# Optimization experiments

Measured on AMD Instinct MI355X. Metric: run time of the kernel, lower is better.

The kernel has to match this reference:

```python
import jax, jax.numpy as jnp
import numpy as np

B, D, T, H, OUT = 256, 256, 256, 512, 256

def setup_inputs() -> dict:
    key = jax.random.key(0)
    ks = jax.random.split(key, 7)
    s = lambda fan: 1.0 / np.sqrt(fan)
    x = jax.random.normal(ks[0], (B, D, T), dtype=jnp.float32)
    Wx = jax.random.normal(ks[1], (D, H), dtype=jnp.float32) * s(D)
    Wh = jax.random.normal(ks[2], (H, H), dtype=jnp.float32) * s(H)
    b = jnp.zeros((H,), dtype=jnp.float32)
    Wout = jax.random.normal(ks[3], (H, OUT), dtype=jnp.float32) * s(H)
    bout = jnp.zeros((OUT,), dtype=jnp.float32)
    init_state = jnp.zeros((1, H), dtype=jnp.float32)  # non-trainable zeros in keras
    return {"x": x, "Wx": Wx, "Wh": Wh, "b": b, "Wout": Wout, "bout": bout, "init_state": init_state}

def reference(x, Wx, Wh, b, Wout, bout, init_state):
    # x: [B, D, T] (time on last axis, as unstacked in the keras layer)
    batch = x.shape[0]
    h0 = jnp.tile(init_state, (batch, 1))              # [B, H]
    xs = jnp.moveaxis(x, -1, 0)                        # [T, B, D]
    # precompute input projections for all steps (hoisted out of the recurrence)
    xproj = jnp.einsum('tbd,dh->tbh', xs, Wx) + b      # [T, B, H]

    def step(h_prev, xp):
        cur = jnp.tanh(xp + h_prev @ Wh)
        # residual: state_i = cell_out + state_{i-1}; at i=0 h_prev is zeros, so always adding is exact
        new = cur + h_prev
        return new, new

    _, states = jax.lax.scan(step, h0, xproj)          # states: [T, B, H]
    states = jnp.moveaxis(states, 0, 1)                # [B, T, H]
    out = states @ Wout + bout                         # [B, T, OUT]
    return out
```

## Files before the change

### kernel.cpp

```cpp
#include <hip/hip_runtime.h>
#include <cstring>
#include <cstdio>

typedef __attribute__((ext_vector_type(8))) short short8;
typedef __attribute__((ext_vector_type(4))) float f32x4;
typedef __attribute__((ext_vector_type(4))) unsigned u32x4;

__device__ __forceinline__ short f2bf(float f){
  unsigned u; __builtin_memcpy(&u, &f, 4);
  u += 0x7FFFu + ((u >> 16) & 1u);
  return (short)(u >> 16);
}
__device__ __forceinline__ float bf2f(short s){
  unsigned u = ((unsigned)(unsigned short)s) << 16;
  float f; __builtin_memcpy(&f, &u, 4);
  return f;
}
__device__ __forceinline__ void split2(float v, short& hi, short& lo){
  hi = f2bf(v);
  float r = v - bf2f(hi);
  lo = f2bf(r);
}
__device__ __forceinline__ unsigned pack2(float v){
  short hi, lo; split2(v, hi, lo);
  return (((unsigned)(unsigned short)hi) << 16) | (unsigned)(unsigned short)lo;
}
__device__ __forceinline__ float tanh_fast(float x){
  float e = __expf(2.0f * x);
  return 1.0f - 2.0f / (e + 1.0f);
}

#define HIDX(r,k) ((((r) * 512) + (k)) ^ (((r) & 7) << 3))

__global__ void transpose_split(const float* __restrict__ in,
                                short* __restrict__ outh, short* __restrict__ outl,
                                int R, int C){
  int idx = blockIdx.x * 256 + threadIdx.x;
  if (idx < R * C){
    int r = idx / C, c = idx % C;
    short h, l; split2(in[(size_t)r * C + c], h, l);
    outh[(size_t)c * R + r] = h;
    outl[(size_t)c * R + r] = l;
  }
}

__global__ void transpose_to_bf16(const float* __restrict__ in, short* __restrict__ out,
                                  int R, int C){
  int idx = blockIdx.x * 256 + threadIdx.x;
  if (idx < R * C){
    int r = idx / C, c = idx % C;
    out[(size_t)c * R + r] = f2bf(in[(size_t)r * C + c]);
  }
}

__global__ __launch_bounds__(256) void transpose_x_split(const float* __restrict__ x,
                                                         short* __restrict__ xTh,
                                                         short* __restrict__ xTl){
  __shared__ float tile[64][65];
  const int b = blockIdx.x, d0 = blockIdx.y * 64, t0 = blockIdx.z * 64;
  const int tid = threadIdx.x;
  const float* xp = x + ((size_t)b * 256 + d0) * 256 + t0;
  for (int v = tid; v < 1024; v += 256){
    int r = v >> 4, c4 = (v & 15) * 4;
    float4 f = *(const float4*)(xp + (size_t)r * 256 + c4);
    tile[r][c4+0] = f.x; tile[r][c4+1] = f.y; tile[r][c4+2] = f.z; tile[r][c4+3] = f.w;
  }
  __syncthreads();
  for (int v = tid; v < 512; v += 256){
    int j = v >> 3, i8 = (v & 7) * 8;
    short8 oh, ol;
    #pragma unroll
    for (int u = 0; u < 8; ++u){ short h, l; split2(tile[i8 + u][j], h, l); oh[u] = h; ol[u] = l; }
    size_t off = ((size_t)(t0 + j) * 256 + b) * 256 + d0 + i8;
    *(short8*)(xTh + off) = oh;
    *(short8*)(xTl + off) = ol;
  }
}

__global__ __launch_bounds__(256) void gemm1_split(
    const short* __restrict__ Ah, const short* __restrict__ Al,
    const short* __restrict__ Bh, const short* __restrict__ Bl,
    const float* __restrict__ bias, float* __restrict__ C0, float* __restrict__ C1,
    int M, int N, int K)
{
  __shared__ short lAh[64][72];
  __shared__ short lAl[64][72];
  __shared__ short lBh[64][72];
  __shared__ short lBl[64][72];
  const int m0 = blockIdx.y * 64, n0 = blockIdx.x * 64;
  const int tid = threadIdx.x;
  const int lane = tid & 63, wave = tid >> 6;
  const int wm = (wave >> 1) * 32, wn = (wave & 1) * 32;
  f32x4 acc[2][2] = {};
  for (int k0 = 0; k0 < K; k0 += 64){
    __syncthreads();
    for (int v = tid; v < 2048; v += 256){
      int sel = v >> 9, idx = v & 511;
      int r = idx >> 3, c = (idx & 7) * 8;
      const short* src = (sel == 0) ? Ah + (size_t)(m0 + r) * K + k0 + c
                       : (sel == 1) ? Al + (size_t)(m0 + r) * K + k0 + c
                       : (sel == 2) ? Bh + (size_t)(n0 + r) * K + k0 + c
                                    : Bl + (size_t)(n0 + r) * K + k0 + c;
      short8 val = *(const short8*)src;
      short* dst = (sel == 0) ? &lAh[r][c] : (sel == 1) ? &lAl[r][c]
                 : (sel == 2) ? &lBh[r][c] : &lBl[r][c];
      *(short8*)dst = val;
    }
    __syncthreads();
    #pragma unroll
    for (int kk = 0; kk < 64; kk += 32){
      int ko = kk + (lane >> 4) * 8;
      short8 ah0 = *(const short8*)&lAh[wm +      (lane & 15)][ko];
      short8 ah1 = *(const short8*)&lAh[wm + 16 + (lane & 15)][ko];
      short8 al0 = *(const short8*)&lAl[wm +      (lane & 15)][ko];
      short8 al1 = *(const short8*)&lAl[wm + 16 + (lane & 15)][ko];
      short8 bh0 = *(const short8*)&lBh[wn +      (lane & 15)][ko];
      short8 bh1 = *(const short8*)&lBh[wn + 16 + (lane & 15)][ko];
      short8 bl0 = *(const short8*)&lBl[wn +      (lane & 15)][ko];
      short8 bl1 = *(const short8*)&lBl[wn + 16 + (lane & 15)][ko];
      acc[0][0] = __builtin_amdgcn_mfma_f32_16x16x32_bf16(ah0, bh0, acc[0][0], 0, 0, 0);
      acc[0][1] = __builtin_amdgcn_mfma_f32_16x16x32_bf16(ah0, bh1, acc[0][1], 0, 0, 0);
      acc[1][0] = __builtin_amdgcn_mfma_f32_16x16x32_bf16(ah1, bh0, acc[1][0], 0, 0, 0);
      acc[1][1] = __builtin_amdgcn_mfma_f32_16x16x32_bf16(ah1, bh1, acc[1][1], 0, 0, 0);
      acc[0][0] = __builtin_amdgcn_mfma_f32_16x16x32_bf16(ah0, bl0, acc[0][0], 0, 0, 0);
      acc[0][1] = __builtin_amdgcn_mfma_f32_16x16x32_bf16(ah0, bl1, acc[0][1], 0, 0, 0);
      acc[1][0] = __builtin_amdgcn_mfma_f32_16x16x32_bf16(ah1, bl0, acc[1][0], 0, 0, 0);
      acc[1][1] = __builtin_amdgcn_mfma_f32_16x16x32_bf16(ah1, bl1, acc[1][1], 0, 0, 0);
      acc[0][0] = __builtin_amdgcn_mfma_f32_16x16x32_bf16(al0, bh0, acc[0][0], 0, 0, 0);
      acc[0][1] = __builtin_amdgcn_mfma_f32_16x16x32_bf16(al0, bh1, acc[0][1], 0, 0, 0);
      acc[1][0] = __builtin_amdgcn_mfma_f32_16x16x32_bf16(al1, bh0, acc[1][0], 0, 0, 0);
      acc[1][1] = __builtin_amdgcn_mfma_f32_16x16x32_bf16(al1, bh1, acc[1][1], 0, 0, 0);
    }
  }
  const int cr = (lane >> 4) * 4, cc = lane & 15;
  #pragma unroll
  for (int i = 0; i < 2; ++i)
  #pragma unroll
  for (int j = 0; j < 2; ++j){
    int row = m0 + wm + i * 16 + cr;
    int col = n0 + wn + j * 16 + cc;
    float bv = bias[col];
    float* base = (row < 32768) ? C0 : C1;
    int rr = (row < 32768) ? row : row - 32768;
    #pragma unroll
    for (int r = 0; r < 4; ++r){
      base[(size_t)(rr + r) * N + col] = acc[i][j][r] + bv;
    }
  }
}

__global__ __launch_bounds__(256, 1) void rnn_steps_v5(
    const float* __restrict__ xp0,
    const float* __restrict__ xp1,
    const short* __restrict__ WhTh,
    const short* __restrict__ WhTl,
    const float* __restrict__ init,
    short* __restrict__ states,
    unsigned* __restrict__ pay,
    unsigned* __restrict__ flags)
{
  __shared__ short hh[16 * 512];
  __shared__ short hl[16 * 512];
  const int tid = threadIdx.x, lane = tid & 63, wave = tid >> 6;
  const int team = blockIdx.x & 31, slice = blockIdx.x >> 5;
  const int b0 = team * 8;
  const int nc = slice * 64 + wave * 16;

  short8 Bh[16], Bl[16];
  {
    const size_t col = (size_t)(nc + (lane & 15));
    const int kb = (lane >> 4) * 8;
    #pragma unroll
    for (int ks = 0; ks < 16; ++ks){
      Bh[ks] = *(const short8*)(WhTh + col * 512 + ks * 32 + kb);
      Bl[ks] = *(const short8*)(WhTl + col * 512 + ks * 32 + kb);
    }
    #pragma unroll
    for (int ks = 0; ks < 16; ++ks){
      asm volatile("" : "+v"(Bh[ks]), "+v"(Bl[ks]));
    }
  }
  for (int v = tid; v < 8 * 512; v += 256){
    int r = 8 + (v >> 9), k = v & 511;
    hh[HIDX(r, k)] = 0; hl[HIDX(r, k)] = 0;
  }
  for (int v = tid; v < 8 * 512; v += 256){
    int r = v >> 9, k = v & 511;
    short hi, lo; split2(init[k], hi, lo);
    hh[HIDX(r, k)] = hi; hl[HIDX(r, k)] = lo;
  }
  __syncthreads();

  const int cc = lane & 15;
  const bool islo = (lane < 32);
  const int mbase = ((lane & 31) >> 4) * 4;
  const int m_0 = mbase + (islo ? 0 : 2);
  const int m_1 = mbase + (islo ? 1 : 3);
  const int n = nc + cc;
  float hr0 = init[n], hr1 = init[n];

  const int am = lane & 15, kb = (lane >> 4) * 8;
  const int rr = tid >> 5, c0 = (tid & 31) * 16;

  for (int t = 0; t < 256; ++t){
    const float* xpb = (t < 128) ? xp0 : xp1;
    const int tt = (t < 128) ? t : t - 128;
    const float xv0 = xpb[((size_t)tt * 256 + b0 + m_0) * 512 + n];
    const float xv1 = xpb[((size_t)tt * 256 + b0 + m_1) * 512 + n];

    if (t > 0){
      const unsigned tagv = (unsigned)t;
      const unsigned* flg = flags + (((size_t)(t & 1)) * 32 + team) * 32;
      u32x4 f0, f1;
      while (true){
        asm volatile("global_load_dwordx4 %0, %1, off sc0 sc1" : "=&v"(f0) : "v"(flg)     : "memory");
        asm volatile("global_load_dwordx4 %0, %1, off sc0 sc1" : "=&v"(f1) : "v"(flg + 4) : "memory");
        asm volatile("s_waitcnt vmcnt(0)" : "+v"(f0), "+v"(f1) :: "memory");
        if (f0.x >= tagv && f0.y >= tagv && f0.z >= tagv && f0.w >= tagv &&
            f1.x >= tagv && f1.y >= tagv && f1.z >= tagv && f1.w >= tagv) break;
        __builtin_amdgcn_s_sleep(1);
      }
      const unsigned* src = pay + ((((size_t)(t & 1)) * 32 + team) * 8 + rr) * 512 + c0;
      u32x4 g0, g1, g2, g3;
      asm volatile("global_load_dwordx4 %0, %1, off sc0 sc1" : "=&v"(g0) : "v"(src +  0) : "memory");
      asm volatile("global_load_dwordx4 %0, %1, off sc0 sc1" : "=&v"(g1) : "v"(src +  4) : "memory");
      asm volatile("global_load_dwordx4 %0, %1, off sc0 sc1" : "=&v"(g2) : "v"(src +  8) : "memory");
      asm volatile("global_load_dwordx4 %0, %1, off sc0 sc1" : "=&v"(g3) : "v"(src + 12) : "memory");
      asm volatile("s_waitcnt vmcnt(0)"
                   : "+v"(g0), "+v"(g1), "+v"(g2), "+v"(g3) :: "memory");
      short8 h0v, h1v, l0v, l1v;
      #pragma unroll
      for (int i = 0; i < 4; ++i){
        unsigned pa = (i < 2) ? ((i == 0) ? g0.x : g0.z) : ((i == 2) ? g1.x : g1.z);
        (void)pa;
      }
      h0v[0] = (short)(g0.x >> 16); h0v[1] = (short)(g0.y >> 16);
      h0v[2] = (short)(g0.z >> 16); h0v[3] = (short)(g0.w >> 16);
      h0v[4] = (short)(g1.x >> 16); h0v[5] = (short)(g1.y >> 16);
      h0v[6] = (short)(g1.z >> 16); h0v[7] = (short)(g1.w >> 16);
      h1v[0] = (short)(g2.x >> 16); h1v[1] = (short)(g2.y >> 16);
      h1v[2] = (short)(g2.z >> 16); h1v[3] = (short)(g2.w >> 16);
      h1v[4] = (short)(g3.x >> 16); h1v[5] = (short)(g3.y >> 16);
      h1v[6] = (short)(g3.z >> 16); h1v[7] = (short)(g3.w >> 16);
      l0v[0] = (short)(g0.x & 0xffffu); l0v[1] = (short)(g0.y & 0xffffu);
      l0v[2] = (short)(g0.z & 0xffffu); l0v[3] = (short)(g0.w & 0xffffu);
      l0v[4] = (short)(g1.x & 0xffffu); l0v[5] = (short)(g1.y & 0xffffu);
      l0v[6] = (short)(g1.z & 0xffffu); l0v[7] = (short)(g1.w & 0xffffu);
      l1v[0] = (short)(g2.x & 0xffffu); l1v[1] = (short)(g2.y & 0xffffu);
      l1v[2] = (short)(g2.z & 0xffffu); l1v[3] = (short)(g2.w & 0xffffu);
      l1v[4] = (short)(g3.x & 0xffffu); l1v[5] = (short)(g3.y & 0xffffu);
      l1v[6] = (short)(g3.z & 0xffffu); l1v[7] = (short)(g3.w & 0xffffu);
      *(short8*)&hh[HIDX(rr, c0)]     = h0v;
      *(short8*)&hh[HIDX(rr, c0 + 8)] = h1v;
      *(short8*)&hl[HIDX(rr, c0)]     = l0v;
      *(short8*)&hl[HIDX(rr, c0 + 8)] = l1v;
      __syncthreads();
    }

    f32x4 ahh = {}, ahl = {}, alh = {};
    #pragma unroll
    for (int ks = 0; ks < 16; ++ks){
      short8 Ah = *(const short8*)&hh[HIDX(am, ks * 32 + kb)];
      short8 Al = *(const short8*)&hl[HIDX(am, ks * 32 + kb)];
      ahh = __builtin_amdgcn_mfma_f32_16x16x32_bf16(Ah, Bh[ks], ahh, 0, 0, 0);
      ahl = __builtin_amdgcn_mfma_f32_16x16x32_bf16(Ah, Bl[ks], ahl, 0, 0, 0);
      alh = __builtin_amdgcn_mfma_f32_16x16x32_bf16(Al, Bh[ks], alh, 0, 0, 0);
    }
    const float s0 = ahh[0] + (ahl[0] + alh[0]);
    const float s1 = ahh[1] + (ahl[1] + alh[1]);
    const float s2 = ahh[2] + (ahl[2] + alh[2]);
    const float s3 = ahh[3] + (ahl[3] + alh[3]);
    const float t2 = __shfl(s2, lane ^ 32);
    const float t3 = __shfl(s3, lane ^ 32);
    const float v0 = islo ? s0 : t2;
    const float v1 = islo ? s1 : t3;

    const float hn0 = tanh_fast(xv0 + v0) + hr0;
    const float hn1 = tanh_fast(xv1 + v1) + hr1;
    hr0 = hn0; hr1 = hn1;

    if (t < 255){
      unsigned* dst = pay + ((((size_t)((t + 1) & 1)) * 32 + team) * 8) * 512;
      unsigned w0 = pack2(hn0), w1 = pack2(hn1);
      unsigned* a0 = dst + (size_t)m_0 * 512 + n;
      unsigned* a1 = dst + (size_t)m_1 * 512 + n;
      asm volatile("global_store_dword %0, %1, off sc0 sc1" :: "v"(a0), "v"(w0) : "memory");
      asm volatile("global_store_dword %0, %1, off sc0 sc1" :: "v"(a1), "v"(w1) : "memory");
    }
    states[((size_t)(b0 + m_0) * 256 + t) * 512 + n] = f2bf(hn0);
    states[((size_t)(b0 + m_1) * 256 + t) * 512 + n] = f2bf(hn1);

    if (t < 255){
      asm volatile("s_waitcnt vmcnt(0)" ::: "memory");
      __syncthreads();
      if (tid == 0){
        unsigned* fdst = flags + (((size_t)((t + 1) & 1)) * 32 + team) * 32 + slice;
        unsigned tagn = (unsigned)(t + 1);
        asm volatile("global_store_dword %0, %1, off sc0 sc1" :: "v"(fdst), "v"(tagn) : "memory");
      }
    }
  }
}

__global__ __launch_bounds__(256) void gemm_bias_f32(
    const short* __restrict__ A, const short* __restrict__ Bt,
    const float* __restrict__ bias, float* __restrict__ C,
    int M, int N, int K)
{
  __shared__ short lA[64][72];
  __shared__ short lB[64][72];
  const int m0 = blockIdx.y * 64, n0 = blockIdx.x * 64;
  const int tid = threadIdx.x;
  const int lane = tid & 63, wave = tid >> 6;
  const int wm = (wave >> 1) * 32, wn = (wave & 1) * 32;
  f32x4 acc[2][2] = {};
  for (int k0 = 0; k0 < K; k0 += 64){
    __syncthreads();
    for (int v = tid; v < 512; v += 256){
      int r = v >> 3, c = v & 7;
      *(short8*)&lA[r][c*8] = *(const short8*)(A + (size_t)(m0 + r) * K + k0 + c*8);
      *(short8*)&lB[r][c*8] = *(const short8*)(Bt + (size_t)(n0 + r) * K + k0 + c*8);
    }
    __syncthreads();
    #pragma unroll
    for (int kk = 0; kk < 64; kk += 32){
      int ko = kk + (lane >> 4) * 8;
      short8 a0 = *(const short8*)&lA[wm +      (lane & 15)][ko];
      short8 a1 = *(const short8*)&lA[wm + 16 + (lane & 15)][ko];
      short8 b0 = *(const short8*)&lB[wn +      (lane & 15)][ko];
      short8 b1 = *(const short8*)&lB[wn + 16 + (lane & 15)][ko];
      acc[0][0] = __builtin_amdgcn_mfma_f32_16x16x32_bf16(a0, b0, acc[0][0], 0, 0, 0);
      acc[0][1] = __builtin_amdgcn_mfma_f32_16x16x32_bf16(a0, b1, acc[0][1], 0, 0, 0);
      acc[1][0] = __builtin_amdgcn_mfma_f32_16x16x32_bf16(a1, b0, acc[1][0], 0, 0, 0);
      acc[1][1] = __builtin_amdgcn_mfma_f32_16x16x32_bf16(a1, b1, acc[1][1], 0, 0, 0);
    }
  }
  const int cr = (lane >> 4) * 4, cc = lane & 15;
  #pragma unroll
  for (int i = 0; i < 2; ++i)
  #pragma unroll
  for (int j = 0; j < 2; ++j){
    int row = m0 + wm + i * 16 + cr;
    int col = n0 + wn + j * 16 + cc;
    float bv = bias[col];
    #pragma unroll
    for (int r = 0; r < 4; ++r){
      C[(size_t)(row + r) * N + col] = acc[i][j][r] + bv;
    }
  }
}

extern "C" void kernel_launch(void* const* d_in, const int* in_sizes, int n_in,
                              void* d_out, int out_size, void* d_ws, size_t ws_size,
                              hipStream_t stream){
  (void)in_sizes; (void)n_in; (void)out_size;
  const float* x    = (const float*)d_in[0];
  const float* Wx   = (const float*)d_in[1];
  const float* Wh   = (const float*)d_in[2];
  const float* bias = (const float*)d_in[3];
  const float* Wout = (const float*)d_in[4];
  const float* bout = (const float*)d_in[5];
  const float* init = (const float*)d_in[6];
  float* out = (float*)d_out;

  char* p = (char*)d_ws;
  short* xTh    = (short*)(p);
  short* xTl    = (short*)(p + 33554432);
  short* states = (short*)(p);
  float* xproj0 = (float*)(p + 67108864);
  float* xproj1 = (float*)d_out;
  short* WxTh   = (short*)(p + 134217728);
  short* WxTl   = (short*)(p + 134479872);
  short* WhTh   = (short*)(p + 134742016);
  short* WhTl   = (short*)(p + 135266304);
  short* WoutT  = (short*)(p + 135790592);
  unsigned* pay   = (unsigned*)(p + 136052736);
  unsigned* flags = (unsigned*)(p + 137101312);
  if (ws_size < 137109504u){
    fprintf(stderr, "kernel_launch: ws_size=%zu < 137109504 needed\n", ws_size);
  }

  hipMemsetAsync(flags, 0, 8192, stream);

  transpose_split<<<(256*512 + 255)/256, 256, 0, stream>>>(Wx, WxTh, WxTl, 256, 512);
  transpose_split<<<(512*512 + 255)/256, 256, 0, stream>>>(Wh, WhTh, WhTl, 512, 512);
  transpose_to_bf16<<<(512*256 + 255)/256, 256, 0, stream>>>(Wout, WoutT, 512, 256);
  transpose_x_split<<<dim3(256, 4, 4), 256, 0, stream>>>(x, xTh, xTl);
  gemm1_split<<<dim3(8, 1024), 256, 0, stream>>>(xTh, xTl, WxTh, WxTl, bias,
                                                 xproj0, xproj1, 65536, 512, 256);
  rnn_steps_v5<<<256, 256, 0, stream>>>(xproj0, xproj1, WhTh, WhTl, init,
                                        states, pay, flags);
  gemm_bias_f32<<<dim3(4, 1024), 256, 0, stream>>>(states, WoutT, bout, out, 65536, 256, 512);
}
```

Measured before the change: 903.9 us.

## Enlarge GEMM tiles to 128x128 and switch RNN barrier to per-wave flags

Both GEMM kernels move from 64x64 to 128x128 block tiles with a 4x4 MFMA accumulator grid per wave, which raises data reuse per LDS load and reduces the block count. The recurrent kernel now has each wave publish its own ready flag right after its payload store, rather than a block-wide syncthreads followed by one flag from thread 0. Consumers poll all flags in parallel across lanes and combine them with a wave vote, without a sleep. The xproj loads are issued asynchronously so they overlap the wait and payload fetch. The larger tiles raise register and LDS pressure, and the finer flags add more spin traffic.

```diff
diff --git a/kernel.cpp b/kernel.cpp
--- a/kernel.cpp
+++ b/kernel.cpp
@@ -83,19 +83,19 @@
     const float* __restrict__ bias, float* __restrict__ C0, float* __restrict__ C1,
     int M, int N, int K)
 {
-  __shared__ short lAh[64][72];
-  __shared__ short lAl[64][72];
-  __shared__ short lBh[64][72];
-  __shared__ short lBl[64][72];
-  const int m0 = blockIdx.y * 64, n0 = blockIdx.x * 64;
+  __shared__ short lAh[128][72];
+  __shared__ short lAl[128][72];
+  __shared__ short lBh[128][72];
+  __shared__ short lBl[128][72];
+  const int m0 = blockIdx.y * 128, n0 = blockIdx.x * 128;
   const int tid = threadIdx.x;
   const int lane = tid & 63, wave = tid >> 6;
-  const int wm = (wave >> 1) * 32, wn = (wave & 1) * 32;
-  f32x4 acc[2][2] = {};
+  const int wm = (wave >> 1) * 64, wn = (wave & 1) * 64;
+  f32x4 acc[4][4] = {};
   for (int k0 = 0; k0 < K; k0 += 64){
     __syncthreads();
-    for (int v = tid; v < 2048; v += 256){
-      int sel = v >> 9, idx = v & 511;
+    for (int v = tid; v < 4096; v += 256){
+      int sel = v >> 10, idx = v & 1023;
       int r = idx >> 3, c = (idx & 7) * 8;
       const short* src = (sel == 0) ? Ah + (size_t)(m0 + r) * K + k0 + c
                        : (sel == 1) ? Al + (size_t)(m0 + r) * K + k0 + c
@@ -110,33 +110,29 @@
     #pragma unroll
     for (int kk = 0; kk < 64; kk += 32){
       int ko = kk + (lane >> 4) * 8;
-      short8 ah0 = *(const short8*)&lAh[wm +      (lane & 15)][ko];
-      short8 ah1 = *(const short8*)&lAh[wm + 16 + (lane & 15)][ko];
-      short8 al0 = *(const short8*)&lAl[wm +      (lane & 15)][ko];
-      short8 al1 = *(const short8*)&lAl[wm + 16 + (lane & 15)][ko];
-      short8 bh0 = *(const short8*)&lBh[wn +      (lane & 15)][ko];
-      short8 bh1 = *(const short8*)&lBh[wn + 16 + (lane & 15)][ko];
-      short8 bl0 = *(const short8*)&lBl[wn +      (lane & 15)][ko];
-      short8 bl1 = *(const short8*)&lBl[wn + 16 + (lane & 15)][ko];
-      acc[0][0] = __builtin_amdgcn_mfma_f32_16x16x32_bf16(ah0, bh0, acc[0][0], 0, 0, 0);
-      acc[0][1] = __builtin_amdgcn_mfma_f32_16x16x32_bf16(ah0, bh1, acc[0][1], 0, 0, 0);
-      acc[1][0] = __builtin_amdgcn_mfma_f32_16x16x32_bf16(ah1, bh0, acc[1][0], 0, 0, 0);
-      acc[1][1] = __builtin_amdgcn_mfma_f32_16x16x32_bf16(ah1, bh1, acc[1][1], 0, 0, 0);
-      acc[0][0] = __builtin_amdgcn_mfma_f32_16x16x32_bf16(ah0, bl0, acc[0][0], 0, 0, 0);
-      acc[0][1] = __builtin_amdgcn_mfma_f32_16x16x32_bf16(ah0, bl1, acc[0][1], 0, 0, 0);
-      acc[1][0] = __builtin_amdgcn_mfma_f32_16x16x32_bf16(ah1, bl0, acc[1][0], 0, 0, 0);
-      acc[1][1] = __builtin_amdgcn_mfma_f32_16x16x32_bf16(ah1, bl1, acc[1][1], 0, 0, 0);
-      acc[0][0] = __builtin_amdgcn_mfma_f32_16x16x32_bf16(al0, bh0, acc[0][0], 0, 0, 0);
-      acc[0][1] = __builtin_amdgcn_mfma_f32_16x16x32_bf16(al0, bh1, acc[0][1], 0, 0, 0);
-      acc[1][0] = __builtin_amdgcn_mfma_f32_16x16x32_bf16(al1, bh0, acc[1][0], 0, 0, 0);
-      acc[1][1] = __builtin_amdgcn_mfma_f32_16x16x32_bf16(al1, bh1, acc[1][1], 0, 0, 0);
+      short8 ah[4], al[4], bh[4], bl[4];
+      #pragma unroll
+      for (int i = 0; i < 4; ++i){
+        ah[i] = *(const short8*)&lAh[wm + i * 16 + (lane & 15)][ko];
+        al[i] = *(const short8*)&lAl[wm + i * 16 + (lane & 15)][ko];
+        bh[i] = *(const short8*)&lBh[wn + i * 16 + (lane & 15)][ko];
+        bl[i] = *(const short8*)&lBl[wn + i * 16 + (lane & 15)][ko];
+      }
+      #pragma unroll
+      for (int i = 0; i < 4; ++i)
+      #pragma unroll
+      for (int j = 0; j < 4; ++j){
+        acc[i][j] = __builtin_amdgcn_mfma_f32_16x16x32_bf16(ah[i], bh[j], acc[i][j], 0, 0, 0);
+        acc[i][j] = __builtin_amdgcn_mfma_f32_16x16x32_bf16(ah[i], bl[j], acc[i][j], 0, 0, 0);
+        acc[i][j] = __builtin_amdgcn_mfma_f32_16x16x32_bf16(al[i], bh[j], acc[i][j], 0, 0, 0);
+      }
     }
   }
   const int cr = (lane >> 4) * 4, cc = lane & 15;
   #pragma unroll
-  for (int i = 0; i < 2; ++i)
+  for (int i = 0; i < 4; ++i)
   #pragma unroll
-  for (int j = 0; j < 2; ++j){
+  for (int j = 0; j < 4; ++j){
     int row = m0 + wm + i * 16 + cr;
     int col = n0 + wn + j * 16 + cc;
     float bv = bias[col];
@@ -149,7 +145,7 @@
   }
 }
 
-__global__ __launch_bounds__(256, 1) void rnn_steps_v5(
+__global__ __launch_bounds__(256, 1) void rnn_steps_v7(
     const float* __restrict__ xp0,
     const float* __restrict__ xp1,
     const short* __restrict__ WhTh,
@@ -169,11 +165,11 @@
   short8 Bh[16], Bl[16];
   {
     const size_t col = (size_t)(nc + (lane & 15));
-    const int kb = (lane >> 4) * 8;
+    const int kb0 = (lane >> 4) * 8;
     #pragma unroll
     for (int ks = 0; ks < 16; ++ks){
-      Bh[ks] = *(const short8*)(WhTh + col * 512 + ks * 32 + kb);
-      Bl[ks] = *(const short8*)(WhTl + col * 512 + ks * 32 + kb);
+      Bh[ks] = *(const short8*)(WhTh + col * 512 + ks * 32 + kb0);
+      Bl[ks] = *(const short8*)(WhTl + col * 512 + ks * 32 + kb0);
     }
     #pragma unroll
     for (int ks = 0; ks < 16; ++ks){
@@ -200,25 +196,22 @@
   float hr0 = init[n], hr1 = init[n];
 
   const int am = lane & 15, kb = (lane >> 4) * 8;
-  const int rr = tid >> 5, c0 = (tid & 31) * 16;
+  const int rr = tid & 7, c0 = ((tid >> 3) & 31) * 16;
 
   for (int t = 0; t < 256; ++t){
-    const float* xpb = (t < 128) ? xp0 : xp1;
-    const int tt = (t < 128) ? t : t - 128;
-    const float xv0 = xpb[((size_t)tt * 256 + b0 + m_0) * 512 + n];
-    const float xv1 = xpb[((size_t)tt * 256 + b0 + m_1) * 512 + n];
-
-    if (t > 0){
+    float xv0, xv1;
+    if (t == 0){
+      xv0 = xp0[(size_t)(b0 + m_0) * 512 + n];
+      xv1 = xp0[(size_t)(b0 + m_1) * 512 + n];
+    } else {
       const unsigned tagv = (unsigned)t;
-      const unsigned* flg = flags + (((size_t)(t & 1)) * 32 + team) * 32;
-      u32x4 f0, f1;
+      const unsigned* flg = flags + (((size_t)(t & 1)) * 32 + team) * 32 + (lane & 7) * 4;
       while (true){
-        asm volatile("global_load_dwordx4 %0, %1, off sc0 sc1" : "=&v"(f0) : "v"(flg)     : "memory");
-        asm volatile("global_load_dwordx4 %0, %1, off sc0 sc1" : "=&v"(f1) : "v"(flg + 4) : "memory");
-        asm volatile("s_waitcnt vmcnt(0)" : "+v"(f0), "+v"(f1) :: "memory");
-        if (f0.x >= tagv && f0.y >= tagv && f0.z >= tagv && f0.w >= tagv &&
-            f1.x >= tagv && f1.y >= tagv && f1.z >= tagv && f1.w >= tagv) break;
-        __builtin_amdgcn_s_sleep(1);
+        u32x4 f;
+        asm volatile("global_load_dwordx4 %0, %1, off sc0 sc1" : "=&v"(f) : "v"(flg) : "memory");
+        asm volatile("s_waitcnt vmcnt(0)" : "+v"(f) :: "memory");
+        bool ok = (f.x >= tagv) && (f.y >= tagv) && (f.z >= tagv) && (f.w >= tagv);
+        if (__all(ok)) break;
       }
       const unsigned* src = pay + ((((size_t)(t & 1)) * 32 + team) * 8 + rr) * 512 + c0;
       u32x4 g0, g1, g2, g3;
@@ -226,14 +219,16 @@
       asm volatile("global_load_dwordx4 %0, %1, off sc0 sc1" : "=&v"(g1) : "v"(src +  4) : "memory");
       asm volatile("global_load_dwordx4 %0, %1, off sc0 sc1" : "=&v"(g2) : "v"(src +  8) : "memory");
       asm volatile("global_load_dwordx4 %0, %1, off sc0 sc1" : "=&v"(g3) : "v"(src + 12) : "memory");
-      asm volatile("s_waitcnt vmcnt(0)"
+      const float* xpb = (t < 128) ? xp0 : xp1;
+      const int tt = (t < 128) ? t : t - 128;
+      const float* xa0 = xpb + ((size_t)tt * 256 + b0 + m_0) * 512 + n;
+      const float* xa1 = xpb + ((size_t)tt * 256 + b0 + m_1) * 512 + n;
+      asm volatile("global_load_dword %0, %1, off" : "=&v"(xv0) : "v"(xa0) : "memory");
+      asm volatile("global_load_dword %0, %1, off" : "=&v"(xv1) : "v"(xa1) : "memory");
+      __syncthreads();
+      asm volatile("s_waitcnt vmcnt(2)"
                    : "+v"(g0), "+v"(g1), "+v"(g2), "+v"(g3) :: "memory");
       short8 h0v, h1v, l0v, l1v;
-      #pragma unroll
-      for (int i = 0; i < 4; ++i){
-        unsigned pa = (i < 2) ? ((i == 0) ? g0.x : g0.z) : ((i == 2) ? g1.x : g1.z);
-        (void)pa;
-      }
       h0v[0] = (short)(g0.x >> 16); h0v[1] = (short)(g0.y >> 16);
       h0v[2] = (short)(g0.z >> 16); h0v[3] = (short)(g0.w >> 16);
       h0v[4] = (short)(g1.x >> 16); h0v[5] = (short)(g1.y >> 16);
@@ -275,6 +270,9 @@
     const float v0 = islo ? s0 : t2;
     const float v1 = islo ? s1 : t3;
 
+    if (t > 0){
+      asm volatile("s_waitcnt vmcnt(0)" : "+v"(xv0), "+v"(xv1) :: "memory");
+    }
     const float hn0 = tanh_fast(xv0 + v0) + hr0;
     const float hn1 = tanh_fast(xv1 + v1) + hr1;
     hr0 = hn0; hr1 = hn1;
@@ -286,19 +284,15 @@
       unsigned* a1 = dst + (size_t)m_1 * 512 + n;
       asm volatile("global_store_dword %0, %1, off sc0 sc1" :: "v"(a0), "v"(w0) : "memory");
       asm volatile("global_store_dword %0, %1, off sc0 sc1" :: "v"(a1), "v"(w1) : "memory");
+      asm volatile("s_waitcnt vmcnt(0)" ::: "memory");
+      if (lane == 0){
+        unsigned* fdst = flags + (((size_t)((t + 1) & 1)) * 32 + team) * 32 + slice * 4 + wave;
+        unsigned tagn = (unsigned)(t + 1);
+        asm volatile("global_store_dword %0, %1, off sc0 sc1" :: "v"(fdst), "v"(tagn) : "memory");
+      }
     }
     states[((size_t)(b0 + m_0) * 256 + t) * 512 + n] = f2bf(hn0);
     states[((size_t)(b0 + m_1) * 256 + t) * 512 + n] = f2bf(hn1);
-
-    if (t < 255){
-      asm volatile("s_waitcnt vmcnt(0)" ::: "memory");
-      __syncthreads();
-      if (tid == 0){
-        unsigned* fdst = flags + (((size_t)((t + 1) & 1)) * 32 + team) * 32 + slice;
-        unsigned tagn = (unsigned)(t + 1);
-        asm volatile("global_store_dword %0, %1, off sc0 sc1" :: "v"(fdst), "v"(tagn) : "memory");
-      }
-    }
   }
 }
 
@@ -307,39 +301,47 @@
     const float* __restrict__ bias, float* __restrict__ C,
     int M, int N, int K)
 {
-  __shared__ short lA[64][72];
-  __shared__ short lB[64][72];
-  const int m0 = blockIdx.y * 64, n0 = blockIdx.x * 64;
+  __shared__ short lA[128][72];
+  __shared__ short lB[128][72];
+  const int m0 = blockIdx.y * 128, n0 = blockIdx.x * 128;
   const int tid = threadIdx.x;
   const int lane = tid & 63, wave = tid >> 6;
-  const int wm = (wave >> 1) * 32, wn = (wave & 1) * 32;
-  f32x4 acc[2][2] = {};
+  const int wm = (wave >> 1) * 64, wn = (wave & 1) * 64;
+  f32x4 acc[4][4] = {};
   for (int k0 = 0; k0 < K; k0 += 64){
     __syncthreads();
-    for (int v = tid; v < 512; v += 256){
-      int r = v >> 3, c = v & 7;
-      *(short8*)&lA[r][c*8] = *(const short8*)(A + (size_t)(m0 + r) * K + k0 + c*8);
-      *(short8*)&lB[r][c*8] = *(const short8*)(Bt + (size_t)(n0 + r) * K + k0 + c*8);
+    for (int v = tid; v < 2048; v += 256){
+      int sel = v >> 10, idx = v & 1023;
+      int r = idx >> 3, c = (idx & 7) * 8;
+      const short* src = (sel == 0) ? A + (size_t)(m0 + r) * K + k0 + c
+                                    : Bt + (size_t)(n0 + r) * K + k0 + c;
+      short8 val = *(const short8*)src;
+      short* dst = (sel == 0) ? &lA[r][c] : &lB[r][c];
+      *(short8*)dst = val;
     }
     __syncthreads();
     #pragma unroll
     for (int kk = 0; kk < 64; kk += 32){
       int ko = kk + (lane >> 4) * 8;
-      short8 a0 = *(const short8*)&lA[wm +      (lane & 15)][ko];
-      short8 a1 = *(const short8*)&lA[wm + 16 + (lane & 15)][ko];
-      short8 b0 = *(const short8*)&lB[wn +      (lane & 15)][ko];
-      short8 b1 = *(const short8*)&lB[wn + 16 + (lane & 15)][ko];
-      acc[0][0] = __builtin_amdgcn_mfma_f32_16x16x32_bf16(a0, b0, acc[0][0], 0, 0, 0);
-      acc[0][1] = __builtin_amdgcn_mfma_f32_16x16x32_bf16(a0, b1, acc[0][1], 0, 0, 0);
-      acc[1][0] = __builtin_amdgcn_mfma_f32_16x16x32_bf16(a1, b0, acc[1][0], 0, 0, 0);
-      acc[1][1] = __builtin_amdgcn_mfma_f32_16x16x32_bf16(a1, b1, acc[1][1], 0, 0, 0);
+      short8 a[4], b[4];
+      #pragma unroll
+      for (int i = 0; i < 4; ++i){
+        a[i] = *(const short8*)&lA[wm + i * 16 + (lane & 15)][ko];
+        b[i] = *(const short8*)&lB[wn + i * 16 + (lane & 15)][ko];
+      }
+      #pragma unroll
+      for (int i = 0; i < 4; ++i)
+      #pragma unroll
+      for (int j = 0; j < 4; ++j){
+        acc[i][j] = __builtin_amdgcn_mfma_f32_16x16x32_bf16(a[i], b[j], acc[i][j], 0, 0, 0);
+      }
     }
   }
   const int cr = (lane >> 4) * 4, cc = lane & 15;
   #pragma unroll
-  for (int i = 0; i < 2; ++i)
+  for (int i = 0; i < 4; ++i)
   #pragma unroll
-  for (int j = 0; j < 2; ++j){
+  for (int j = 0; j < 4; ++j){
     int row = m0 + wm + i * 16 + cr;
     int col = n0 + wn + j * 16 + cc;
     float bv = bias[col];
@@ -386,9 +388,9 @@
   transpose_split<<<(512*512 + 255)/256, 256, 0, stream>>>(Wh, WhTh, WhTl, 512, 512);
   transpose_to_bf16<<<(512*256 + 255)/256, 256, 0, stream>>>(Wout, WoutT, 512, 256);
   transpose_x_split<<<dim3(256, 4, 4), 256, 0, stream>>>(x, xTh, xTl);
-  gemm1_split<<<dim3(8, 1024), 256, 0, stream>>>(xTh, xTl, WxTh, WxTl, bias,
-                                                 xproj0, xproj1, 65536, 512, 256);
-  rnn_steps_v5<<<256, 256, 0, stream>>>(xproj0, xproj1, WhTh, WhTl, init,
+  gemm1_split<<<dim3(4, 512), 256, 0, stream>>>(xTh, xTl, WxTh, WxTl, bias,
+                                                xproj0, xproj1, 65536, 512, 256);
+  rnn_steps_v7<<<256, 256, 0, stream>>>(xproj0, xproj1, WhTh, WhTl, init,
                                         states, pay, flags);
-  gemm_bias_f32<<<dim3(4, 1024), 256, 0, stream>>>(states, WoutT, bout, out, 65536, 256, 512);
-}
+  gemm_bias_f32<<<dim3(2, 512), 256, 0, stream>>>(states, WoutT, bout, out, 65536, 256, 512);
+}
```

Result: slower. 1.004 ms (+11.1%).
